# Optimization experiments

Hardware: AMD Instinct MI355X
Metric: run time of the kernel (lower is better)

## Reference

```python
import jax, jax.numpy as jnp
import numpy as np

# Gather3d sparse-mode constants derived from CausalConv3d(kernel=3, stride=1, padding=1)
BLOCK = (16, 16)   # block_size (b0, b1)
OFFSET = (1, 1)    # conv.spatial_padding (pad_h, pad_w)
PAD_T = 2          # conv.time_padding = 2 * padding[0]


def setup_inputs() -> dict:
    key = jax.random.key(0)
    k1, k2 = jax.random.split(key)
    x = jax.random.normal(k1, (1, 128, 16, 128, 128), dtype=jnp.float32)
    active_indices = jax.random.randint(k2, (128, 2), 0, 112, dtype=jnp.int32)
    return {"x": x, "active_indices": active_indices}


def reference(x, active_indices):
    b, c, t, H, W = x.shape
    bh, bw = BLOCK
    ph, pw = OFFSET
    # F.pad(x, (pad_w, block_w, pad_h, block_h, pad_t, 0)) in torch (last dims first)
    padded = jnp.pad(x, ((0, 0), (0, 0), (PAD_T, 0), (ph, bh), (pw, bw)))

    def take(idx):
        # slice of shape [b, c, t+PAD_T, bh, bw] starting at (idx_y+pad_h, idx_x+pad_w)
        return jax.lax.dynamic_slice(
            padded,
            (0, 0, 0, idx[0] + ph, idx[1] + pw),
            (b, c, t + PAD_T, bh, bw),
        )

    blocks = jax.vmap(take)(active_indices)          # [N, b, c, T, bh, bw]
    n = active_indices.shape[0]
    # torch.stack(blocks, dim=1) -> [b, N, ...] -> view(b*N, ...)
    out = jnp.swapaxes(blocks, 0, 1).reshape(b * n, c, t + PAD_T, bh, bw)
    return out
```

## Files before the change

### kernel.cpp

```cpp
#include <hip/hip_runtime.h>

#define C_DIM 128
#define T_DIM 16
#define H_DIM 128
#define W_DIM 128
#define PAD_T 2
#define TT (T_DIM + PAD_T)
#define CPB 2
#define F4_PER_CHUNK (TT * 64)
#define F4_PER_BLOCK (CPB * F4_PER_CHUNK)
#define ITERS (F4_PER_BLOCK / 256)

typedef float f4u __attribute__((ext_vector_type(4), aligned(4)));
typedef float f4a __attribute__((ext_vector_type(4), aligned(16)));

__global__ __launch_bounds__(256) void gather3d_kernel(
    const float* __restrict__ x,
    const int*   __restrict__ active_idx,
    float*       __restrict__ out)
{
    const int cbase = blockIdx.x * CPB;
    const int n     = blockIdx.y;

    const int idx0 = active_idx[2 * n];
    const int idx1 = active_idx[2 * n + 1];

    f4a* outb = (f4a*)(out + ((size_t)n * C_DIM + cbase) * (size_t)(TT * 256));

    #pragma unroll
    for (int it = 0; it < ITERS; ++it) {
        const int w     = threadIdx.x + it * 256;
        const int plane = w >> 6;
        const int local = w & 63;
        const int cl    = (plane >= TT) ? 1 : 0;
        const int tt    = plane - cl * TT;
        const int i     = local >> 2;
        const int j     = (local & 3) << 2;

        f4a v = {0.f, 0.f, 0.f, 0.f};
        if (tt >= PAD_T) {
            const float* src = x
                + (((size_t)(cbase + cl) * T_DIM + (size_t)(tt - PAD_T)) * H_DIM
                   + (size_t)(idx0 + i)) * W_DIM
                + idx1 + j;
            v = *(const f4u*)src;
        }
        __builtin_nontemporal_store(v, outb + w);
    }
}

extern "C" void kernel_launch(void* const* d_in, const int* in_sizes, int n_in,
                              void* d_out, int out_size, void* d_ws, size_t ws_size,
                              hipStream_t stream) {
    const float* x   = (const float*)d_in[0];
    const int*   idx = (const int*)d_in[1];
    float*       out = (float*)d_out;

    const int N = in_sizes[1] / 2;

    dim3 grid(C_DIM / CPB, N);
    dim3 block(256);
    gather3d_kernel<<<grid, block, 0, stream>>>(x, idx, out);
}
```

Baseline: 435.5 us.

## Stage each input plane in LDS and emit all gathered blocks per plane

Each workgroup now handles one (channel, time) plane. It loads the whole 128x128 plane once into padded LDS, then loops over all N active indices and writes each 16x16 tile from LDS with scalar nontemporal stores. Before, every output tile re-read its source from global memory, so overlapping tiles were fetched many times; now the input is read only once. In exchange, each block uses about 74KB of LDS, stores shrink from float4 to scalar, and the per-n loop is serial within each block.

```diff
diff --git a/kernel.cpp b/kernel.cpp
--- a/kernel.cpp
+++ b/kernel.cpp
@@ -6,46 +6,57 @@
 #define W_DIM 128
 #define PAD_T 2
 #define TT (T_DIM + PAD_T)
-#define CPB 2
-#define F4_PER_CHUNK (TT * 64)
-#define F4_PER_BLOCK (CPB * F4_PER_CHUNK)
-#define ITERS (F4_PER_BLOCK / 256)
 
-typedef float f4u __attribute__((ext_vector_type(4), aligned(4)));
-typedef float f4a __attribute__((ext_vector_type(4), aligned(16)));
+#define S_LDS 144
+#define PLANE_F (H_DIM * S_LDS)
 
-__global__ __launch_bounds__(256) void gather3d_kernel(
+typedef float f4 __attribute__((ext_vector_type(4), aligned(16)));
+
+__global__ __launch_bounds__(256, 2) void gather3d_plane(
     const float* __restrict__ x,
     const int*   __restrict__ active_idx,
-    float*       __restrict__ out)
+    float*       __restrict__ out,
+    int N)
 {
-    const int cbase = blockIdx.x * CPB;
-    const int n     = blockIdx.y;
+    __shared__ float plane[PLANE_F];
 
-    const int idx0 = active_idx[2 * n];
-    const int idx1 = active_idx[2 * n + 1];
+    const int c   = blockIdx.x;
+    const int tt  = blockIdx.y;
+    const int tid = threadIdx.x;
 
-    f4a* outb = (f4a*)(out + ((size_t)n * C_DIM + cbase) * (size_t)(TT * 256));
+    if (tt >= PAD_T) {
+        const float* __restrict__ src =
+            x + ((size_t)c * T_DIM + (size_t)(tt - PAD_T)) * (size_t)(H_DIM * W_DIM);
+        #pragma unroll
+        for (int it = 0; it < (H_DIM * W_DIM) / (256 * 4); ++it) {
+            const int f   = (it * 256 + tid) * 4;
+            const int r   = f >> 7;
+            const int col = f & 127;
+            *(f4*)(&plane[r * S_LDS + col]) = *(const f4*)(src + f);
+        }
+    }
+    __syncthreads();
 
-    #pragma unroll
-    for (int it = 0; it < ITERS; ++it) {
-        const int w     = threadIdx.x + it * 256;
-        const int plane = w >> 6;
-        const int local = w & 63;
-        const int cl    = (plane >= TT) ? 1 : 0;
-        const int tt    = plane - cl * TT;
-        const int i     = local >> 2;
-        const int j     = (local & 3) << 2;
+    const int row = tid >> 4;
+    const int col = tid & 15;
+    float*       op      = out + ((size_t)c * TT + tt) * 256 + tid;
+    const size_t ostride = (size_t)C_DIM * TT * 256;
 
-        f4a v = {0.f, 0.f, 0.f, 0.f};
-        if (tt >= PAD_T) {
-            const float* src = x
-                + (((size_t)(cbase + cl) * T_DIM + (size_t)(tt - PAD_T)) * H_DIM
-                   + (size_t)(idx0 + i)) * W_DIM
-                + idx1 + j;
-            v = *(const f4u*)src;
+    if (tt >= PAD_T) {
+        const float* pl = plane + row * S_LDS + col;
+        #pragma unroll 4
+        for (int n = 0; n < N; ++n) {
+            const int i0 = active_idx[2 * n];
+            const int i1 = active_idx[2 * n + 1];
+            __builtin_nontemporal_store(pl[i0 * S_LDS + i1], op);
+            op += ostride;
         }
-        __builtin_nontemporal_store(v, outb + w);
+    } else {
+        #pragma unroll 4
+        for (int n = 0; n < N; ++n) {
+            __builtin_nontemporal_store(0.0f, op);
+            op += ostride;
+        }
     }
 }
 
@@ -58,7 +69,6 @@
 
     const int N = in_sizes[1] / 2;
 
-    dim3 grid(C_DIM / CPB, N);
-    dim3 block(256);
-    gather3d_kernel<<<grid, block, 0, stream>>>(x, idx, out);
+    dim3 grid(C_DIM, TT);
+    gather3d_plane<<<grid, dim3(256), 0, stream>>>(x, idx, out, N);
 }
```

After: 401.0 us. -7.9%, faster.

## Restructure gather so each wave streams four full channels per workgroup

Applied to the files above, without the earlier changes.

Each workgroup now covers 16 channels instead of 2. Every wave walks 4 channels sequentially, writing two zero planes followed by 16 unrolled time planes, which gives fewer, larger workgroups and removes the per-element plane/channel index math. Nontemporal stores are replaced with ordinary stores, and launch bounds now hint at 4 waves per SIMD. The risk is less parallelism across the grid (1024 workgroups) and the loss of nontemporal hints for the large output write stream.

```diff
diff --git a/kernel.cpp b/kernel.cpp
--- a/kernel.cpp
+++ b/kernel.cpp
@@ -6,46 +6,50 @@
 #define W_DIM 128
 #define PAD_T 2
 #define TT (T_DIM + PAD_T)
-#define CPB 2
-#define F4_PER_CHUNK (TT * 64)
-#define F4_PER_BLOCK (CPB * F4_PER_CHUNK)
-#define ITERS (F4_PER_BLOCK / 256)
 
+#define C_PER_WG   16
+#define C_PER_WAVE 4
+
+typedef float f4  __attribute__((ext_vector_type(4), aligned(16)));
 typedef float f4u __attribute__((ext_vector_type(4), aligned(4)));
-typedef float f4a __attribute__((ext_vector_type(4), aligned(16)));
 
-__global__ __launch_bounds__(256) void gather3d_kernel(
+__global__ __launch_bounds__(256, 4) void gather3d_nmajor(
     const float* __restrict__ x,
     const int*   __restrict__ active_idx,
-    float*       __restrict__ out)
+    float*       __restrict__ out,
+    int N)
 {
-    const int cbase = blockIdx.x * CPB;
+    const int chunk = blockIdx.x;
     const int n     = blockIdx.y;
+    const int tid   = threadIdx.x;
+    const int wid   = tid >> 6;
+    const int lane  = tid & 63;
+    const int r     = lane >> 2;
+    const int q     = (lane & 3) << 2;
 
-    const int idx0 = active_idx[2 * n];
-    const int idx1 = active_idx[2 * n + 1];
+    const int i0 = active_idx[2 * n];
+    const int i1 = active_idx[2 * n + 1];
 
-    f4a* outb = (f4a*)(out + ((size_t)n * C_DIM + cbase) * (size_t)(TT * 256));
+    const int c0 = chunk * C_PER_WG + wid * C_PER_WAVE;
 
-    #pragma unroll
-    for (int it = 0; it < ITERS; ++it) {
-        const int w     = threadIdx.x + it * 256;
-        const int plane = w >> 6;
-        const int local = w & 63;
-        const int cl    = (plane >= TT) ? 1 : 0;
-        const int tt    = plane - cl * TT;
-        const int i     = local >> 2;
-        const int j     = (local & 3) << 2;
+    float* op = out + ((size_t)n * C_DIM + c0) * (size_t)(TT * 256)
+                    + r * 16 + q;
 
-        f4a v = {0.f, 0.f, 0.f, 0.f};
-        if (tt >= PAD_T) {
-            const float* src = x
-                + (((size_t)(cbase + cl) * T_DIM + (size_t)(tt - PAD_T)) * H_DIM
-                   + (size_t)(idx0 + i)) * W_DIM
-                + idx1 + j;
-            v = *(const f4u*)src;
+    const float* xp = x + (((size_t)c0 * T_DIM) * H_DIM + (size_t)(i0 + r)) * W_DIM
+                        + i1 + q;
+
+    const f4 z = {0.f, 0.f, 0.f, 0.f};
+
+    for (int cc = 0; cc < C_PER_WAVE; ++cc) {
+        *(f4*)op = z;  op += 256;
+        *(f4*)op = z;  op += 256;
+        #pragma unroll
+        for (int t = 0; t < T_DIM; ++t) {
+            f4 v = *(const f4u*)(xp + (size_t)t * (H_DIM * W_DIM));
+            *(f4*)op = v;
+            op += 256;
         }
-        __builtin_nontemporal_store(v, outb + w);
+        xp += (size_t)T_DIM * H_DIM * W_DIM;
     }
 }
 
@@ -58,7 +62,6 @@
 
     const int N = in_sizes[1] / 2;
 
-    dim3 grid(C_DIM / CPB, N);
-    dim3 block(256);
-    gather3d_kernel<<<grid, block, 0, stream>>>(x, idx, out);
+    dim3 grid(C_DIM / C_PER_WG, N);
+    gather3d_nmajor<<<grid, dim3(256), 0, stream>>>(x, idx, out, N);
 }
```

Result: no change. 442.9 us (+1.7%).
